# Performance work log

Hardware: AMD Instinct MI355X
Metric: run time of the kernel (lower is better)

The kernel has to match this reference:

```python
import jax, jax.numpy as jnp
import numpy as np

B, S, D, H, L, V, DFF = 2, 2048, 1024, 16, 4, 32000, 4096
DH = D // H
STD = 0.02
EPS = 1e-5


def _sinusoidal_pe(seq_len, d_model):
    pos = np.arange(seq_len)[:, None].astype(np.float32)
    div = np.exp(np.arange(0, d_model, 2).astype(np.float32) * (-np.log(10000.0) / d_model))
    pe = np.zeros((seq_len, d_model), dtype=np.float32)
    pe[:, 0::2] = np.sin(pos * div)
    pe[:, 1::2] = np.cos(pos * div)
    return jnp.asarray(pe)


def _layernorm(x, g, b):
    mu = jnp.mean(x, axis=-1, keepdims=True)
    var = jnp.mean(jnp.square(x - mu), axis=-1, keepdims=True)
    return (x - mu) * jax.lax.rsqrt(var + EPS) * g + b


def setup_inputs() -> dict:
    key = jax.random.key(0)
    ks = jax.random.split(key, 12)
    input_ids = jax.random.randint(ks[0], (B, S), 0, V)
    tok_emb = STD * jax.random.normal(ks[1], (V, D), dtype=jnp.float32)
    tok_emb = tok_emb.at[0].set(0.0)  # padding_idx=0 zeroed
    Wq = STD * jax.random.normal(ks[2], (L, D, D), dtype=jnp.float32)
    Wk = STD * jax.random.normal(ks[3], (L, D, D), dtype=jnp.float32)
    Wv = STD * jax.random.normal(ks[4], (L, D, D), dtype=jnp.float32)
    Wo = STD * jax.random.normal(ks[5], (L, D, D), dtype=jnp.float32)
    W1 = STD * jax.random.normal(ks[6], (L, D, DFF), dtype=jnp.float32)
    W2 = STD * jax.random.normal(ks[7], (L, DFF, D), dtype=jnp.float32)
    Wout = STD * jax.random.normal(ks[8], (D, V), dtype=jnp.float32)
    zD = jnp.zeros((L, D), dtype=jnp.float32)
    return {
        'input_ids': input_ids, 'tok_emb': tok_emb,
        'Wq': Wq, 'bq': zD, 'Wk': Wk, 'bk': zD, 'Wv': Wv, 'bv': zD, 'Wo': Wo, 'bo': zD,
        'ln1_g': jnp.ones((L, D), jnp.float32), 'ln1_b': zD,
        'W1': W1, 'b1': jnp.zeros((L, DFF), jnp.float32), 'W2': W2, 'b2': zD,
        'ln3_g': jnp.ones((L, D), jnp.float32), 'ln3_b': zD,
        'Wout': Wout, 'bout': jnp.zeros((V,), jnp.float32),
    }


def reference(input_ids, tok_emb, Wq, bq, Wk, bk, Wv, bv, Wo, bo,
              ln1_g, ln1_b, W1, b1, W2, b2, ln3_g, ln3_b, Wout, bout):
    pe = _sinusoidal_pe(S, D)
    causal = jnp.tril(jnp.ones((S, S), dtype=bool))  # [S,S]
    x = tok_emb[input_ids] * jnp.float32(np.sqrt(D)) + pe  # [B,S,D]
    scale = jnp.float32(1.0 / np.sqrt(DH))
    for l in range(L):
        q = (x @ Wq[l] + bq[l]).reshape(B, S, H, DH).transpose(0, 2, 1, 3)
        k = (x @ Wk[l] + bk[l]).reshape(B, S, H, DH).transpose(0, 2, 1, 3)
        v = (x @ Wv[l] + bv[l]).reshape(B, S, H, DH).transpose(0, 2, 1, 3)
        scores = jnp.einsum('bhqd,bhkd->bhqk', q, k) * scale
        scores = jnp.where(causal, scores, jnp.float32(-1e9))
        attn = jax.nn.softmax(scores, axis=-1)
        o = jnp.einsum('bhqk,bhkd->bhqd', attn, v)
        o = o.transpose(0, 2, 1, 3).reshape(B, S, D) @ Wo[l] + bo[l]
        x = _layernorm(x + o, ln1_g[l], ln1_b[l])
        f = jax.nn.relu(x @ W1[l] + b1[l]) @ W2[l] + b2[l]
        x = _layernorm(x + f, ln3_g[l], ln3_b[l])
    logits = x @ Wout + bout  # [B,S,V]
    return logits
```

## Files before the change

### kernel.cpp

```cpp
#include <hip/hip_runtime.h>
#include <stdint.h>

typedef unsigned short u16;
typedef __attribute__((ext_vector_type(8))) short bf16x8;
typedef __attribute__((ext_vector_type(4))) float f32x4;

#define NB 2
#define NS 2048
#define ND 1024
#define NH 16
#define NL 4
#define NV 32000
#define NF 4096
#define NDH 64
#define NM (NB*NS)

__device__ __forceinline__ u16 f2b(float f) {
  union { float f; uint32_t u; } v; v.f = f;
  uint32_t r = v.u + 0x7FFFu + ((v.u >> 16) & 1u);
  return (u16)(r >> 16);
}

#define GLOAD_LDS16(gp, lp) __builtin_amdgcn_global_load_lds( \
    (const __attribute__((address_space(1))) void*)(gp), \
    (__attribute__((address_space(3))) void*)(lp), 16, 0, 0)

#define VMCNT8 do { asm volatile("s_waitcnt vmcnt(8)" ::: "memory"); __builtin_amdgcn_sched_barrier(0); } while (0)
#define VMCNT0 do { asm volatile("s_waitcnt vmcnt(0)" ::: "memory"); __builtin_amdgcn_sched_barrier(0); } while (0)
#define LGKM0  do { asm volatile("s_waitcnt lgkmcnt(0)" ::: "memory"); __builtin_amdgcn_sched_barrier(0); } while (0)

__global__ __launch_bounds__(256)
void k_transpose_convert(const float* __restrict__ w, u16* __restrict__ wt, int K, int N) {
  __shared__ float tile[32][33];
  int n0 = blockIdx.x * 32;
  int k0 = blockIdx.y * 32;
  int tx = threadIdx.x & 31;
  int ty = threadIdx.x >> 5;
#pragma unroll
  for (int i = 0; i < 4; i++) {
    int kk = ty + i * 8;
    tile[kk][tx] = w[(size_t)(k0 + kk) * N + (n0 + tx)];
  }
  __syncthreads();
#pragma unroll
  for (int i = 0; i < 4; i++) {
    int nn = ty + i * 8;
    wt[(size_t)(n0 + nn) * K + (k0 + tx)] = f2b(tile[tx][nn]);
  }
}

__global__ __launch_bounds__(256)
void k_embed(const int* __restrict__ ids, const float* __restrict__ emb,
             float* __restrict__ x, u16* __restrict__ xb) {
  int row = blockIdx.x;
  int s = row & (NS - 1);
  int tok = ids[row];
  const float* e = emb + (size_t)tok * ND;
  int d0 = threadIdx.x * 4;
  float y[4];
#pragma unroll
  for (int j = 0; j < 4; j++) {
    int dd = d0 + j;
    float di = (float)(dd & ~1);
    float dv = expf(di * (-9.210340371976184f / (float)ND));
    float ang = (float)s * dv;
    float pe = (dd & 1) ? cosf(ang) : sinf(ang);
    y[j] = e[dd] * 32.0f + pe;
  }
  float4 w; w.x = y[0]; w.y = y[1]; w.z = y[2]; w.w = y[3];
  *(float4*)(x + (size_t)row * ND + d0) = w;
  uint2 pk;
  pk.x = (uint32_t)f2b(y[0]) | ((uint32_t)f2b(y[1]) << 16);
  pk.y = (uint32_t)f2b(y[2]) | ((uint32_t)f2b(y[3]) << 16);
  *(uint2*)(xb + (size_t)row * ND + d0) = pk;
}

__global__ __launch_bounds__(256)
void k_ln(const float* __restrict__ xin, const float* __restrict__ add,
          const float* __restrict__ g, const float* __restrict__ bb,
          float* __restrict__ xout, u16* __restrict__ xbout) {
  int row = blockIdx.x;
  int t = threadIdx.x;
  const float4 xi = *(const float4*)(xin + (size_t)row * ND + t * 4);
  const float4 ai = *(const float4*)(add + (size_t)row * ND + t * 4);
  float v0 = xi.x + ai.x, v1 = xi.y + ai.y, v2 = xi.z + ai.z, v3 = xi.w + ai.w;
  float s = v0 + v1 + v2 + v3;
  float s2 = v0 * v0 + v1 * v1 + v2 * v2 + v3 * v3;
#pragma unroll
  for (int d = 32; d >= 1; d >>= 1) { s += __shfl_xor(s, d); s2 += __shfl_xor(s2, d); }
  __shared__ float rs[8];
  int w = t >> 6;
  if ((t & 63) == 0) { rs[w] = s; rs[4 + w] = s2; }
  __syncthreads();
  s = rs[0] + rs[1] + rs[2] + rs[3];
  s2 = rs[4] + rs[5] + rs[6] + rs[7];
  float mu = s * (1.0f / ND);
  float var = s2 * (1.0f / ND) - mu * mu;
  float rr = rsqrtf(var + 1e-5f);
  const float4 gg = *(const float4*)(g + t * 4);
  const float4 be = *(const float4*)(bb + t * 4);
  float y0 = (v0 - mu) * rr * gg.x + be.x;
  float y1 = (v1 - mu) * rr * gg.y + be.y;
  float y2 = (v2 - mu) * rr * gg.z + be.z;
  float y3 = (v3 - mu) * rr * gg.w + be.w;
  float4 yo; yo.x = y0; yo.y = y1; yo.z = y2; yo.w = y3;
  *(float4*)(xout + (size_t)row * ND + t * 4) = yo;
  uint2 pk;
  pk.x = (uint32_t)f2b(y0) | ((uint32_t)f2b(y1) << 16);
  pk.y = (uint32_t)f2b(y2) | ((uint32_t)f2b(y3) << 16);
  *(uint2*)(xbout + (size_t)row * ND + t * 4) = pk;
}

template<int MODE>
__global__ __launch_bounds__(256)
void k_gemm_bt(const u16* __restrict__ A, const u16* __restrict__ Bt,
               const float* __restrict__ bias0, const float* __restrict__ bias1,
               const float* __restrict__ bias2,
               float* __restrict__ Cf, u16* __restrict__ Cb,
               int M, int N, int K, float scale) {
  constexpr int BM = 128, BN = 128, BK = 32;
  __shared__ __align__(16) u16 As[2][BM * BK];
  __shared__ __align__(16) u16 Bs[2][BN * BK];

  const int tid = threadIdx.x;
  const int lane = tid & 63;
  const int wave = tid >> 6;

  const int bm = blockIdx.x * BM;
  const int bn = blockIdx.y * BN;

  const int wr = (wave >> 1) * 64;
  const int wc = (wave & 1) * 64;
  const int lr = lane & 15;
  const int lk = (lane >> 4) * 8;

  const u16* Abase = A + (size_t)bm * K;
  const u16* Bbase = Bt + (size_t)bn * K;
  const int srow = lane >> 2;
  const int scol = (lane & 3) * 8;

  auto stage = [&](int buf, int kt) {
    const u16* Ag = Abase + (size_t)kt * BK + scol;
    const u16* Bg = Bbase + (size_t)kt * BK + scol;
#pragma unroll
    for (int i = 0; i < 2; i++) {
      const int rbase = (i * 4 + wave) * 16;
      GLOAD_LDS16(Ag + (size_t)(rbase + srow) * K, &As[buf][rbase * BK]);
      GLOAD_LDS16(Bg + (size_t)(rbase + srow) * K, &Bs[buf][rbase * BK]);
    }
  };

  f32x4 acc[4][4] = {};
  const int nk = K / BK;
  stage(0, 0);
  for (int kt = 0; kt < nk; ++kt) {
    __syncthreads();
    if (kt + 1 < nk) stage((kt + 1) & 1, kt + 1);
    const int buf = kt & 1;
    bf16x8 af[4], bfv[4];
#pragma unroll
    for (int m = 0; m < 4; m++)
      af[m] = *(const bf16x8*)(&As[buf][(wr + m * 16 + lr) * BK + lk]);
#pragma unroll
    for (int n = 0; n < 4; n++)
      bfv[n] = *(const bf16x8*)(&Bs[buf][(wc + n * 16 + lr) * BK + lk]);
#pragma unroll
    for (int m = 0; m < 4; m++)
#pragma unroll
      for (int n = 0; n < 4; n++)
        acc[m][n] = __builtin_amdgcn_mfma_f32_16x16x32_bf16(af[m], bfv[n], acc[m][n], 0, 0, 0);
  }

  const int lg = lane >> 4;
#pragma unroll
  for (int m = 0; m < 4; m++) {
#pragma unroll
    for (int n = 0; n < 4; n++) {
      int col = bn + wc + n * 16 + lr;
      float bv;
      if (MODE == 3) {
        int which = col >> 10;
        int cc = col & 1023;
        const float* bp = (which == 0) ? bias0 : ((which == 1) ? bias1 : bias2);
        bv = bp[cc];
      } else {
        bv = bias0[col];
      }
      if (MODE == 3 && (col >> 10) == 2) {
        int cc = col & 1023;
        int row0 = bm + wr + m * 16 + lg * 4;
        int b_ = row0 >> 11;
        int s_ = row0 & (NS - 1);
        int h_ = cc >> 6;
        int dh = cc & 63;
        ushort4 pk;
        pk.x = f2b(acc[m][n][0] + bv);
        pk.y = f2b(acc[m][n][1] + bv);
        pk.z = f2b(acc[m][n][2] + bv);
        pk.w = f2b(acc[m][n][3] + bv);
        *(ushort4*)(Cb + (size_t)2 * NM * ND +
                    ((((size_t)b_ * NH + h_) * NDH) + dh) * NS + s_) = pk;
        continue;
      }
#pragma unroll
      for (int j = 0; j < 4; j++) {
        int row = bm + wr + m * 16 + lg * 4 + j;
        float v = acc[m][n][j] + bv;
        if (MODE == 0) {
          Cf[(size_t)row * N + col] = v;
        } else if (MODE == 1) {
          Cb[(size_t)row * N + col] = f2b(fmaxf(v, 0.0f));
        } else {
          int which = col >> 10;
          int cc = col & 1023;
          if (which == 0) v *= scale;
          int b_ = row >> 11;
          int s_ = row & (NS - 1);
          int h_ = cc >> 6;
          int dh = cc & 63;
          Cb[(size_t)which * ((size_t)NM * ND) +
             ((((size_t)b_ * NH + h_) * NS) + s_) * NDH + dh] = f2b(v);
        }
      }
    }
  }
}

template<int MODE>
__global__ __launch_bounds__(512, 2)
void k_gemm256(const u16* __restrict__ A, const u16* __restrict__ Bt,
               const float* __restrict__ bias,
               float* __restrict__ Cf, u16* __restrict__ Cb,
               int M, int N, int K) {
  __shared__ __align__(16) u16 As2[2][256 * 64];
  __shared__ __align__(16) u16 Bs2[2][256 * 64];

  const int tid = threadIdx.x;
  const int lane = tid & 63;
  const int wave = tid >> 6;
  const int wrM = wave >> 2;
  const int wcN = wave & 3;
  const int lr = lane & 15;
  const int g = lane >> 4;
  const int r7 = lr & 7;

  const int bm = blockIdx.x * 256;
  const int bn = blockIdx.y * 256;

  const int srow_in = lane >> 3;
  const int schunk = lane & 7;
  const int sq = (schunk ^ srow_in) * 8;

  auto stageT = [&](int buf, int t) {
#pragma unroll
    for (int s = 0; s < 4; ++s) {
      const int rbase = (s * 8 + wave) * 8;
      const int row = rbase + srow_in;
      GLOAD_LDS16(A + (size_t)(bm + row) * K + t * 64 + sq, &As2[buf][rbase * 64]);
      GLOAD_LDS16(Bt + (size_t)(bn + row) * K + t * 64 + sq, &Bs2[buf][rbase * 64]);
    }
  };

  f32x4 acc[8][4] = {};
  const int NT = K / 64;

  stageT(0, 0);
  stageT(1, 1);

  for (int t = 0; t < NT; ++t) {
    const int buf = t & 1;
    if (t == NT - 1) { VMCNT0; } else { VMCNT8; }
    __builtin_amdgcn_s_barrier();

    const char* ab = (const char*)(&As2[buf][0]);
    const char* bb = (const char*)(&Bs2[buf][0]);
    bf16x8 aF[8], bF[4];
#pragma unroll
    for (int n = 0; n < 4; n++) {
      int row = wcN * 64 + n * 16 + lr;
      bF[n] = *(const bf16x8*)(bb + row * 128 + ((g ^ r7) * 16));
    }
#pragma unroll
    for (int m = 0; m < 8; m++) {
      int row = wrM * 128 + m * 16 + lr;
      aF[m] = *(const bf16x8*)(ab + row * 128 + ((g ^ r7) * 16));
    }
    __builtin_amdgcn_s_setprio(1);
#pragma unroll
    for (int m = 0; m < 8; m++)
#pragma unroll
      for (int n = 0; n < 4; n++)
        acc[m][n] = __builtin_amdgcn_mfma_f32_16x16x32_bf16(aF[m], bF[n], acc[m][n], 0, 0, 0);
    __builtin_amdgcn_s_setprio(0);

    bf16x8 aG[8], bG[4];
#pragma unroll
    for (int n = 0; n < 4; n++) {
      int row = wcN * 64 + n * 16 + lr;
      bG[n] = *(const bf16x8*)(bb + row * 128 + (((4 + g) ^ r7) * 16));
    }
#pragma unroll
    for (int m = 0; m < 8; m++) {
      int row = wrM * 128 + m * 16 + lr;
      aG[m] = *(const bf16x8*)(ab + row * 128 + (((4 + g) ^ r7) * 16));
    }
    LGKM0;
    __builtin_amdgcn_s_barrier();
    if (t + 2 < NT) stageT(buf, t + 2);
    __builtin_amdgcn_s_setprio(1);
#pragma unroll
    for (int m = 0; m < 8; m++)
#pragma unroll
      for (int n = 0; n < 4; n++)
        acc[m][n] = __builtin_amdgcn_mfma_f32_16x16x32_bf16(aG[m], bG[n], acc[m][n], 0, 0, 0);
    __builtin_amdgcn_s_setprio(0);
  }

#pragma unroll
  for (int m = 0; m < 8; m++) {
#pragma unroll
    for (int n = 0; n < 4; n++) {
      int col = bn + wcN * 64 + n * 16 + lr;
      float bv = bias[col];
#pragma unroll
      for (int j = 0; j < 4; j++) {
        int row = bm + wrM * 128 + m * 16 + g * 4 + j;
        float v = acc[m][n][j] + bv;
        if (MODE == 0) Cf[(size_t)row * N + col] = v;
        else           Cb[(size_t)row * N + col] = f2b(fmaxf(v, 0.0f));
      }
    }
  }
}

__global__ __launch_bounds__(256)
void k_attn(const u16* __restrict__ Q, const u16* __restrict__ Kq,
            const u16* __restrict__ Vt, u16* __restrict__ O) {
  const int qt = blockIdx.x;
  const int bh = blockIdx.y;
  const int b_ = bh >> 4, h_ = bh & 15;
  const int tid = threadIdx.x, lane = tid & 63, wave = tid >> 6;
  const int lr = lane & 15, lg = lane >> 4;

  __shared__ __align__(16) u16 Ks[64 * 64];
  __shared__ __align__(16) u16 Vs[64 * 64];
  __shared__ __align__(16) u16 Ps[4][16 * 64];

  const size_t base = (size_t)bh * NS * NDH;
  bf16x8 qf0, qf1;
  {
    const u16* qp = Q + base + (size_t)(qt * 64 + wave * 16 + lr) * NDH;
    qf0 = *(const bf16x8*)(qp + lg * 8);
    qf1 = *(const bf16x8*)(qp + 32 + lg * 8);
  }

  const int idx0 = tid, idx1 = tid + 256;
  const int r0 = idx0 >> 3, r1 = idx1 >> 3;
  const int c0 = (idx0 & 7) * 8, c1 = (idx1 & 7) * 8;
  const int so0 = r0 * 128 + ((c0 * 2) ^ ((r0 & 7) << 4));
  const int so1 = r1 * 128 + ((c1 * 2) ^ ((r1 & 7) << 4));

  bf16x8 rk0, rk1, rv0, rv1;
  auto loadregs = [&](int kt2) {
    const u16* Kg = Kq + base + (size_t)(kt2 * 64) * NDH;
    const u16* Vg = Vt + base + kt2 * 64;
    rk0 = *(const bf16x8*)(Kg + (size_t)r0 * NDH + c0);
    rk1 = *(const bf16x8*)(Kg + (size_t)r1 * NDH + c1);
    rv0 = *(const bf16x8*)(Vg + (size_t)r0 * NS + c0);
    rv1 = *(const bf16x8*)(Vg + (size_t)r1 * NS + c1);
  };

  float mrun[4] = {-1e30f, -1e30f, -1e30f, -1e30f};
  float lrun[4] = {0.f, 0.f, 0.f, 0.f};
  f32x4 oacc[4] = {};
  const int q0 = qt * 64 + wave * 16;

  loadregs(0);
  for (int kt2 = 0; kt2 <= qt; ++kt2) {
    *(bf16x8*)((char*)Ks + so0) = rk0;
    *(bf16x8*)((char*)Ks + so1) = rk1;
    *(bf16x8*)((char*)Vs + so0) = rv0;
    *(bf16x8*)((char*)Vs + so1) = rv1;
    __syncthreads();
    if (kt2 < qt) loadregs(kt2 + 1);

    f32x4 sc[4];
    __builtin_amdgcn_s_setprio(1);
#pragma unroll
    for (int c = 0; c < 4; c++) {
      int row = c * 16 + lr;
      const char* kp = (const char*)Ks + row * 128;
      int sm = (row & 7) << 4;
      bf16x8 k0 = *(const bf16x8*)(kp + ((lg * 16) ^ sm));
      bf16x8 k1 = *(const bf16x8*)(kp + ((64 + lg * 16) ^ sm));
      f32x4 s = {};
      s = __builtin_amdgcn_mfma_f32_16x16x32_bf16(qf0, k0, s, 0, 0, 0);
      s = __builtin_amdgcn_mfma_f32_16x16x32_bf16(qf1, k1, s, 0, 0, 0);
      sc[c] = s;
    }
    __builtin_amdgcn_s_setprio(0);

    if (kt2 == qt) {
#pragma unroll
      for (int c = 0; c < 4; c++)
#pragma unroll
        for (int j = 0; j < 4; j++) {
          int qg = q0 + lg * 4 + j;
          int kg = qt * 64 + c * 16 + lr;
          if (kg > qg) sc[c][j] = -1e9f;
        }
    }

#pragma unroll
    for (int j = 0; j < 4; j++) {
      float mt = fmaxf(fmaxf(sc[0][j], sc[1][j]), fmaxf(sc[2][j], sc[3][j]));
#pragma unroll
      for (int d = 8; d >= 1; d >>= 1) mt = fmaxf(mt, __shfl_xor(mt, d));
      float mnew = fmaxf(mrun[j], mt);
      float corr = __expf(mrun[j] - mnew);
      float ps = 0.f;
#pragma unroll
      for (int c = 0; c < 4; c++) {
        float p = __expf(sc[c][j] - mnew);
        sc[c][j] = p;
        ps += p;
      }
#pragma unroll
      for (int d = 8; d >= 1; d >>= 1) ps += __shfl_xor(ps, d);
      lrun[j] = lrun[j] * corr + ps;
      mrun[j] = mnew;
#pragma unroll
      for (int n = 0; n < 4; n++) oacc[n][j] *= corr;
    }

    char* pw = (char*)Ps[wave];
#pragma unroll
    for (int c = 0; c < 4; c++)
#pragma unroll
      for (int j = 0; j < 4; j++) {
        int row = lg * 4 + j;
        *(u16*)(pw + row * 128 + ((((c * 16 + lr) * 2)) ^ ((row & 7) << 4))) = f2b(sc[c][j]);
      }

    {
      int smq = (lr & 7) << 4;
      bf16x8 pa0 = *(const bf16x8*)(pw + lr * 128 + ((lg * 16) ^ smq));
      bf16x8 pa1 = *(const bf16x8*)(pw + lr * 128 + ((64 + lg * 16) ^ smq));
      __builtin_amdgcn_s_setprio(1);
#pragma unroll
      for (int n = 0; n < 4; n++) {
        int row = n * 16 + lr;
        const char* vp = (const char*)Vs + row * 128;
        int sm = (row & 7) << 4;
        bf16x8 v0 = *(const bf16x8*)(vp + ((lg * 16) ^ sm));
        bf16x8 v1 = *(const bf16x8*)(vp + ((64 + lg * 16) ^ sm));
        oacc[n] = __builtin_amdgcn_mfma_f32_16x16x32_bf16(pa0, v0, oacc[n], 0, 0, 0);
        oacc[n] = __builtin_amdgcn_mfma_f32_16x16x32_bf16(pa1, v1, oacc[n], 0, 0, 0);
      }
      __builtin_amdgcn_s_setprio(0);
    }
    __syncthreads();
  }

#pragma unroll
  for (int j = 0; j < 4; j++) {
    float inv = 1.0f / lrun[j];
    int s_ = qt * 64 + wave * 16 + lg * 4 + j;
    size_t orow = ((size_t)b_ * NS + s_) * ND + h_ * NDH;
#pragma unroll
    for (int n = 0; n < 4; n++)
      O[orow + n * 16 + lr] = f2b(oacc[n][j] * inv);
  }
}

extern "C" void kernel_launch(void* const* d_in, const int* in_sizes, int n_in,
                              void* d_out, int out_size, void* d_ws, size_t ws_size,
                              hipStream_t stream) {
  const int* ids = (const int*)d_in[0];
  const float* tok_emb = (const float*)d_in[1];
  const float* Wq = (const float*)d_in[2];
  const float* bq = (const float*)d_in[3];
  const float* Wk = (const float*)d_in[4];
  const float* bk = (const float*)d_in[5];
  const float* Wv = (const float*)d_in[6];
  const float* bv = (const float*)d_in[7];
  const float* Wo = (const float*)d_in[8];
  const float* bo = (const float*)d_in[9];
  const float* ln1g = (const float*)d_in[10];
  const float* ln1b = (const float*)d_in[11];
  const float* W1 = (const float*)d_in[12];
  const float* b1 = (const float*)d_in[13];
  const float* W2 = (const float*)d_in[14];
  const float* b2 = (const float*)d_in[15];
  const float* ln3g = (const float*)d_in[16];
  const float* ln3b = (const float*)d_in[17];
  const float* Wout = (const float*)d_in[18];
  const float* bout = (const float*)d_in[19];
  float* out = (float*)d_out;

  char* ws = (char*)d_ws;
  size_t off = 0;
  auto alloc = [&](size_t bytes) -> void* {
    void* p = ws + off;
    off += (bytes + 255) & ~(size_t)255;
    return p;
  };
  float* x    = (float*)alloc((size_t)NM * ND * 4);
  float* tmp  = (float*)alloc((size_t)NM * ND * 4);
  u16* xb     = (u16*)alloc((size_t)NM * ND * 2);
  u16* hb     = (u16*)alloc((size_t)NM * NF * 2);
  u16* qkvb   = (u16*)alloc((size_t)3 * NM * ND * 2);
  u16* ob     = (u16*)alloc((size_t)NM * ND * 2);
  u16* Wqkvt  = (u16*)alloc((size_t)NL * 3 * ND * ND * 2);
  u16* Wot    = (u16*)alloc((size_t)NL * ND * ND * 2);
  u16* W1t    = (u16*)alloc((size_t)NL * (size_t)NF * ND * 2);
  u16* W2t    = (u16*)alloc((size_t)NL * (size_t)ND * NF * 2);
  u16* Woutt  = (u16*)alloc((size_t)NV * ND * 2);

  for (int l = 0; l < NL; l++) {
    size_t wl = (size_t)l * ND * ND;
    u16* qkvl = Wqkvt + (size_t)l * 3 * ND * ND;
    dim3 gdd(ND / 32, ND / 32);
    k_transpose_convert<<<gdd, 256, 0, stream>>>(Wq + wl, qkvl, ND, ND);
    k_transpose_convert<<<gdd, 256, 0, stream>>>(Wk + wl, qkvl + (size_t)ND * ND, ND, ND);
    k_transpose_convert<<<gdd, 256, 0, stream>>>(Wv + wl, qkvl + (size_t)2 * ND * ND, ND, ND);
    k_transpose_convert<<<gdd, 256, 0, stream>>>(Wo + wl, Wot + wl, ND, ND);
    k_transpose_convert<<<dim3(NF / 32, ND / 32), 256, 0, stream>>>(
        W1 + (size_t)l * ND * NF, W1t + (size_t)l * (size_t)NF * ND, ND, NF);
    k_transpose_convert<<<dim3(ND / 32, NF / 32), 256, 0, stream>>>(
        W2 + (size_t)l * NF * ND, W2t + (size_t)l * (size_t)ND * NF, NF, ND);
  }
  k_transpose_convert<<<dim3(NV / 32, ND / 32), 256, 0, stream>>>(Wout, Woutt, ND, NV);

  k_embed<<<NM, 256, 0, stream>>>(ids, tok_emb, x, xb);

  for (int l = 0; l < NL; l++) {
    size_t wl = (size_t)l * ND * ND;
    u16* qkvl = Wqkvt + (size_t)l * 3 * ND * ND;

    k_gemm_bt<3><<<dim3(NM / 128, 3 * ND / 128), 256, 0, stream>>>(
        xb, qkvl, bq + l * ND, bk + l * ND, bv + l * ND,
        nullptr, qkvb, NM, 3 * ND, ND, 0.125f);

    k_attn<<<dim3(NS / 64, NB * NH), 256, 0, stream>>>(
        qkvb, qkvb + (size_t)NM * ND, qkvb + (size_t)2 * NM * ND, ob);

    k_gemm_bt<0><<<dim3(NM / 128, ND / 128), 256, 0, stream>>>(
        ob, Wot + wl, bo + l * ND, nullptr, nullptr, tmp, nullptr, NM, ND, ND, 1.0f);

    k_ln<<<NM, 256, 0, stream>>>(x, tmp, ln1g + l * ND, ln1b + l * ND, x, xb);

    k_gemm256<1><<<dim3(NM / 256, NF / 256), 512, 0, stream>>>(
        xb, W1t + (size_t)l * (size_t)NF * ND, b1 + l * NF, nullptr, hb, NM, NF, ND);

    k_gemm_bt<0><<<dim3(NM / 128, ND / 128), 256, 0, stream>>>(
        hb, W2t + (size_t)l * (size_t)ND * NF, b2 + l * ND, nullptr, nullptr,
        tmp, nullptr, NM, ND, NF, 1.0f);

    k_ln<<<NM, 256, 0, stream>>>(x, tmp, ln3g + l * ND, ln3b + l * ND, x, xb);
  }

  k_gemm256<0><<<dim3(NM / 256, NV / 256), 512, 0, stream>>>(
      xb, Woutt, bout, out, nullptr, NM, NV, ND);
}
```

Before: 1.882 ms.

## Restructure 256-tile GEMM into quadrant phases and enlarge attention query tile

The 256x256 GEMM main loop is split into four quadrant phases. Each phase loads only the A/B fragments it needs, uses extra barriers, and interleaves the next-tile A and B global-to-LDS stages between MFMA phases, which lowers register pressure and spreads memory issue. The attention kernel now processes 128 queries per block (32 per wave), so each K/V tile staged in LDS is reused by twice as many queries and half as many blocks are launched. It also adds a lazy softmax rescale that skips the correction unless the running max grows by more than 8. The trade-offs are more barriers in the GEMM, coarser causal load balancing in attention, and fewer attention blocks to fill the GPU.

```diff
diff --git a/kernel.cpp b/kernel.cpp
--- a/kernel.cpp
+++ b/kernel.cpp
@@ -28,6 +28,7 @@
 #define VMCNT8 do { asm volatile("s_waitcnt vmcnt(8)" ::: "memory"); __builtin_amdgcn_sched_barrier(0); } while (0)
 #define VMCNT0 do { asm volatile("s_waitcnt vmcnt(0)" ::: "memory"); __builtin_amdgcn_sched_barrier(0); } while (0)
 #define LGKM0  do { asm volatile("s_waitcnt lgkmcnt(0)" ::: "memory"); __builtin_amdgcn_sched_barrier(0); } while (0)
+#define MFMA16(a,b,c) __builtin_amdgcn_mfma_f32_16x16x32_bf16((a),(b),(c),0,0,0)
 
 __global__ __launch_bounds__(256)
 void k_transpose_convert(const float* __restrict__ w, u16* __restrict__ wt, int K, int N) {
@@ -168,7 +169,7 @@
     for (int m = 0; m < 4; m++)
 #pragma unroll
       for (int n = 0; n < 4; n++)
-        acc[m][n] = __builtin_amdgcn_mfma_f32_16x16x32_bf16(af[m], bfv[n], acc[m][n], 0, 0, 0);
+        acc[m][n] = MFMA16(af[m], bfv[n], acc[m][n]);
   }
 
   const int lg = lane >> 4;
@@ -251,69 +252,112 @@
   const int schunk = lane & 7;
   const int sq = (schunk ^ srow_in) * 8;
 
-  auto stageT = [&](int buf, int t) {
-#pragma unroll
-    for (int s = 0; s < 4; ++s) {
-      const int rbase = (s * 8 + wave) * 8;
-      const int row = rbase + srow_in;
-      GLOAD_LDS16(A + (size_t)(bm + row) * K + t * 64 + sq, &As2[buf][rbase * 64]);
-      GLOAD_LDS16(Bt + (size_t)(bn + row) * K + t * 64 + sq, &Bs2[buf][rbase * 64]);
+  auto stageA = [&](int buf, int t) {
+#pragma unroll
+    for (int s2 = 0; s2 < 4; ++s2) {
+      const int rbase = (s2 * 8 + wave) * 8;
+      GLOAD_LDS16(A + (size_t)(bm + rbase + srow_in) * K + t * 64 + sq, &As2[buf][rbase * 64]);
+    }
+  };
+  auto stageB = [&](int buf, int t) {
+#pragma unroll
+    for (int s2 = 0; s2 < 4; ++s2) {
+      const int rbase = (s2 * 8 + wave) * 8;
+      GLOAD_LDS16(Bt + (size_t)(bn + rbase + srow_in) * K + t * 64 + sq, &Bs2[buf][rbase * 64]);
     }
   };
 
   f32x4 acc[8][4] = {};
   const int NT = K / 64;
 
-  stageT(0, 0);
-  stageT(1, 1);
+  stageA(0, 0); stageB(0, 0);
+  stageA(1, 1); stageB(1, 1);
 
   for (int t = 0; t < NT; ++t) {
     const int buf = t & 1;
-    if (t == NT - 1) { VMCNT0; } else { VMCNT8; }
+    if (t + 1 < NT) { VMCNT8; } else { VMCNT0; }
     __builtin_amdgcn_s_barrier();
 
     const char* ab = (const char*)(&As2[buf][0]);
-    const char* bb = (const char*)(&Bs2[buf][0]);
-    bf16x8 aF[8], bF[4];
-#pragma unroll
-    for (int n = 0; n < 4; n++) {
+    const char* bb2 = (const char*)(&Bs2[buf][0]);
+    bf16x8 aF[4][2], bF[4][2];
+
+#pragma unroll
+    for (int m = 0; m < 4; m++) {
+      int row = wrM * 128 + m * 16 + lr;
+      aF[m][0] = *(const bf16x8*)(ab + row * 128 + ((g ^ r7) * 16));
+      aF[m][1] = *(const bf16x8*)(ab + row * 128 + (((4 + g) ^ r7) * 16));
+    }
+#pragma unroll
+    for (int n = 0; n < 2; n++) {
       int row = wcN * 64 + n * 16 + lr;
-      bF[n] = *(const bf16x8*)(bb + row * 128 + ((g ^ r7) * 16));
-    }
-#pragma unroll
-    for (int m = 0; m < 8; m++) {
-      int row = wrM * 128 + m * 16 + lr;
-      aF[m] = *(const bf16x8*)(ab + row * 128 + ((g ^ r7) * 16));
-    }
+      bF[n][0] = *(const bf16x8*)(bb2 + row * 128 + ((g ^ r7) * 16));
+      bF[n][1] = *(const bf16x8*)(bb2 + row * 128 + (((4 + g) ^ r7) * 16));
+    }
+    __builtin_amdgcn_s_barrier();
+    LGKM0;
     __builtin_amdgcn_s_setprio(1);
 #pragma unroll
-    for (int m = 0; m < 8; m++)
-#pragma unroll
-      for (int n = 0; n < 4; n++)
-        acc[m][n] = __builtin_amdgcn_mfma_f32_16x16x32_bf16(aF[m], bF[n], acc[m][n], 0, 0, 0);
+    for (int m = 0; m < 4; m++)
+#pragma unroll
+      for (int n = 0; n < 2; n++) {
+        acc[m][n] = MFMA16(aF[m][0], bF[n][0], acc[m][n]);
+        acc[m][n] = MFMA16(aF[m][1], bF[n][1], acc[m][n]);
+      }
     __builtin_amdgcn_s_setprio(0);
-
-    bf16x8 aG[8], bG[4];
-#pragma unroll
-    for (int n = 0; n < 4; n++) {
+    __builtin_amdgcn_s_barrier();
+
+#pragma unroll
+    for (int n = 2; n < 4; n++) {
       int row = wcN * 64 + n * 16 + lr;
-      bG[n] = *(const bf16x8*)(bb + row * 128 + (((4 + g) ^ r7) * 16));
-    }
-#pragma unroll
-    for (int m = 0; m < 8; m++) {
-      int row = wrM * 128 + m * 16 + lr;
-      aG[m] = *(const bf16x8*)(ab + row * 128 + (((4 + g) ^ r7) * 16));
-    }
+      bF[n][0] = *(const bf16x8*)(bb2 + row * 128 + ((g ^ r7) * 16));
+      bF[n][1] = *(const bf16x8*)(bb2 + row * 128 + (((4 + g) ^ r7) * 16));
+    }
+    __builtin_amdgcn_s_barrier();
     LGKM0;
-    __builtin_amdgcn_s_barrier();
-    if (t + 2 < NT) stageT(buf, t + 2);
     __builtin_amdgcn_s_setprio(1);
 #pragma unroll
-    for (int m = 0; m < 8; m++)
-#pragma unroll
-      for (int n = 0; n < 4; n++)
-        acc[m][n] = __builtin_amdgcn_mfma_f32_16x16x32_bf16(aG[m], bG[n], acc[m][n], 0, 0, 0);
+    for (int m = 0; m < 4; m++)
+#pragma unroll
+      for (int n = 2; n < 4; n++) {
+        acc[m][n] = MFMA16(aF[m][0], bF[n][0], acc[m][n]);
+        acc[m][n] = MFMA16(aF[m][1], bF[n][1], acc[m][n]);
+      }
     __builtin_amdgcn_s_setprio(0);
+    __builtin_amdgcn_s_barrier();
+
+#pragma unroll
+    for (int m = 0; m < 4; m++) {
+      int row = wrM * 128 + (m + 4) * 16 + lr;
+      aF[m][0] = *(const bf16x8*)(ab + row * 128 + ((g ^ r7) * 16));
+      aF[m][1] = *(const bf16x8*)(ab + row * 128 + (((4 + g) ^ r7) * 16));
+    }
+    if (t + 2 < NT) stageB(buf, t + 2);
+    __builtin_amdgcn_s_barrier();
+    LGKM0;
+    __builtin_amdgcn_s_setprio(1);
+#pragma unroll
+    for (int m = 0; m < 4; m++)
+#pragma unroll
+      for (int n = 0; n < 2; n++) {
+        acc[m + 4][n] = MFMA16(aF[m][0], bF[n][0], acc[m + 4][n]);
+        acc[m + 4][n] = MFMA16(aF[m][1], bF[n][1], acc[m + 4][n]);
+      }
+    __builtin_amdgcn_s_setprio(0);
+    __builtin_amdgcn_s_barrier();
+
+    if (t + 2 < NT) stageA(buf, t + 2);
+    __builtin_amdgcn_s_barrier();
+    __builtin_amdgcn_s_setprio(1);
+#pragma unroll
+    for (int m = 0; m < 4; m++)
+#pragma unroll
+      for (int n = 2; n < 4; n++) {
+        acc[m + 4][n] = MFMA16(aF[m][0], bF[n][0], acc[m + 4][n]);
+        acc[m + 4][n] = MFMA16(aF[m][1], bF[n][1], acc[m + 4][n]);
+      }
+    __builtin_amdgcn_s_setprio(0);
+    __builtin_amdgcn_s_barrier();
   }
 
 #pragma unroll
@@ -344,14 +388,15 @@
 
   __shared__ __align__(16) u16 Ks[64 * 64];
   __shared__ __align__(16) u16 Vs[64 * 64];
-  __shared__ __align__(16) u16 Ps[4][16 * 64];
+  __shared__ __align__(16) u16 Ps[4][32 * 64];
 
   const size_t base = (size_t)bh * NS * NDH;
-  bf16x8 qf0, qf1;
-  {
-    const u16* qp = Q + base + (size_t)(qt * 64 + wave * 16 + lr) * NDH;
-    qf0 = *(const bf16x8*)(qp + lg * 8);
-    qf1 = *(const bf16x8*)(qp + 32 + lg * 8);
+  bf16x8 qf[2][2];
+#pragma unroll
+  for (int mf = 0; mf < 2; mf++) {
+    const u16* qp = Q + base + (size_t)(qt * 128 + wave * 32 + mf * 16 + lr) * NDH;
+    qf[mf][0] = *(const bf16x8*)(qp + lg * 8);
+    qf[mf][1] = *(const bf16x8*)(qp + 32 + lg * 8);
   }
 
   const int idx0 = tid, idx1 = tid + 256;
@@ -370,82 +415,119 @@
     rv1 = *(const bf16x8*)(Vg + (size_t)r1 * NS + c1);
   };
 
-  float mrun[4] = {-1e30f, -1e30f, -1e30f, -1e30f};
-  float lrun[4] = {0.f, 0.f, 0.f, 0.f};
-  f32x4 oacc[4] = {};
-  const int q0 = qt * 64 + wave * 16;
+  float mrun[2][4], lrun[2][4];
+  f32x4 oacc[2][4] = {};
+#pragma unroll
+  for (int mf = 0; mf < 2; mf++)
+#pragma unroll
+    for (int j = 0; j < 4; j++) { mrun[mf][j] = -1e30f; lrun[mf][j] = 0.f; }
+
+  const int qmin = qt * 128 + wave * 32;
+  const int qmax = qmin + 31;
+  const int nkv = 2 * qt + 2;
 
   loadregs(0);
-  for (int kt2 = 0; kt2 <= qt; ++kt2) {
+  for (int kt2 = 0; kt2 < nkv; ++kt2) {
     *(bf16x8*)((char*)Ks + so0) = rk0;
     *(bf16x8*)((char*)Ks + so1) = rk1;
     *(bf16x8*)((char*)Vs + so0) = rv0;
     *(bf16x8*)((char*)Vs + so1) = rv1;
     __syncthreads();
-    if (kt2 < qt) loadregs(kt2 + 1);
-
-    f32x4 sc[4];
-    __builtin_amdgcn_s_setprio(1);
-#pragma unroll
-    for (int c = 0; c < 4; c++) {
-      int row = c * 16 + lr;
-      const char* kp = (const char*)Ks + row * 128;
-      int sm = (row & 7) << 4;
-      bf16x8 k0 = *(const bf16x8*)(kp + ((lg * 16) ^ sm));
-      bf16x8 k1 = *(const bf16x8*)(kp + ((64 + lg * 16) ^ sm));
-      f32x4 s = {};
-      s = __builtin_amdgcn_mfma_f32_16x16x32_bf16(qf0, k0, s, 0, 0, 0);
-      s = __builtin_amdgcn_mfma_f32_16x16x32_bf16(qf1, k1, s, 0, 0, 0);
-      sc[c] = s;
-    }
-    __builtin_amdgcn_s_setprio(0);
-
-    if (kt2 == qt) {
-#pragma unroll
-      for (int c = 0; c < 4; c++)
+    if (kt2 + 1 < nkv) loadregs(kt2 + 1);
+
+    const bool active = (kt2 * 64 <= qmax);
+    if (active) {
+      f32x4 sc[2][4];
+      __builtin_amdgcn_s_setprio(1);
+#pragma unroll
+      for (int c = 0; c < 4; c++) {
+        int row = c * 16 + lr;
+        const char* kp = (const char*)Ks + row * 128;
+        int sm = (row & 7) << 4;
+        bf16x8 k0 = *(const bf16x8*)(kp + ((lg * 16) ^ sm));
+        bf16x8 k1 = *(const bf16x8*)(kp + ((64 + lg * 16) ^ sm));
+#pragma unroll
+        for (int mf = 0; mf < 2; mf++) {
+          f32x4 s = {};
+          s = MFMA16(qf[mf][0], k0, s);
+          s = MFMA16(qf[mf][1], k1, s);
+          sc[mf][c] = s;
+        }
+      }
+      __builtin_amdgcn_s_setprio(0);
+
+      if (kt2 * 64 + 63 > qmin) {
+#pragma unroll
+        for (int mf = 0; mf < 2; mf++)
+#pragma unroll
+          for (int c = 0; c < 4; c++)
+#pragma unroll
+            for (int j = 0; j < 4; j++) {
+              int qg = qmin + mf * 16 + lg * 4 + j;
+              int kg = kt2 * 64 + c * 16 + lr;
+              if (kg > qg) sc[mf][c][j] = -1e9f;
+            }
+      }
+
+      float mt[2][4];
+      float dmax = -1e30f;
+#pragma unroll
+      for (int mf = 0; mf < 2; mf++)
 #pragma unroll
         for (int j = 0; j < 4; j++) {
-          int qg = q0 + lg * 4 + j;
-          int kg = qt * 64 + c * 16 + lr;
-          if (kg > qg) sc[c][j] = -1e9f;
+          float m0 = fmaxf(fmaxf(sc[mf][0][j], sc[mf][1][j]), fmaxf(sc[mf][2][j], sc[mf][3][j]));
+#pragma unroll
+          for (int d = 8; d >= 1; d >>= 1) m0 = fmaxf(m0, __shfl_xor(m0, d));
+          mt[mf][j] = m0;
+          dmax = fmaxf(dmax, m0 - mrun[mf][j]);
         }
-    }
-
-#pragma unroll
-    for (int j = 0; j < 4; j++) {
-      float mt = fmaxf(fmaxf(sc[0][j], sc[1][j]), fmaxf(sc[2][j], sc[3][j]));
-#pragma unroll
-      for (int d = 8; d >= 1; d >>= 1) mt = fmaxf(mt, __shfl_xor(mt, d));
-      float mnew = fmaxf(mrun[j], mt);
-      float corr = __expf(mrun[j] - mnew);
-      float ps = 0.f;
-#pragma unroll
-      for (int c = 0; c < 4; c++) {
-        float p = __expf(sc[c][j] - mnew);
-        sc[c][j] = p;
-        ps += p;
-      }
-#pragma unroll
-      for (int d = 8; d >= 1; d >>= 1) ps += __shfl_xor(ps, d);
-      lrun[j] = lrun[j] * corr + ps;
-      mrun[j] = mnew;
-#pragma unroll
-      for (int n = 0; n < 4; n++) oacc[n][j] *= corr;
-    }
-
-    char* pw = (char*)Ps[wave];
-#pragma unroll
-    for (int c = 0; c < 4; c++)
-#pragma unroll
-      for (int j = 0; j < 4; j++) {
-        int row = lg * 4 + j;
-        *(u16*)(pw + row * 128 + ((((c * 16 + lr) * 2)) ^ ((row & 7) << 4))) = f2b(sc[c][j]);
-      }
-
-    {
-      int smq = (lr & 7) << 4;
-      bf16x8 pa0 = *(const bf16x8*)(pw + lr * 128 + ((lg * 16) ^ smq));
-      bf16x8 pa1 = *(const bf16x8*)(pw + lr * 128 + ((64 + lg * 16) ^ smq));
+      const bool need = __any(dmax > 8.0f);
+
+#pragma unroll
+      for (int mf = 0; mf < 2; mf++)
+#pragma unroll
+        for (int j = 0; j < 4; j++) {
+          float mold = mrun[mf][j];
+          float mnew = need ? fmaxf(mold, mt[mf][j]) : mold;
+          float ps = 0.f;
+#pragma unroll
+          for (int c = 0; c < 4; c++) {
+            float p = __expf(sc[mf][c][j] - mnew);
+            sc[mf][c][j] = p;
+            ps += p;
+          }
+#pragma unroll
+          for (int d = 8; d >= 1; d >>= 1) ps += __shfl_xor(ps, d);
+          if (need) {
+            float corr = __expf(mold - mnew);
+            lrun[mf][j] = lrun[mf][j] * corr + ps;
+            mrun[mf][j] = mnew;
+#pragma unroll
+            for (int n = 0; n < 4; n++) oacc[mf][n][j] *= corr;
+          } else {
+            lrun[mf][j] += ps;
+          }
+        }
+
+      char* pw = (char*)Ps[wave];
+#pragma unroll
+      for (int mf = 0; mf < 2; mf++)
+#pragma unroll
+        for (int c = 0; c < 4; c++)
+#pragma unroll
+          for (int j = 0; j < 4; j++) {
+            int row = mf * 16 + lg * 4 + j;
+            *(u16*)(pw + row * 128 + ((((c * 16 + lr) * 2)) ^ ((row & 7) << 4))) = f2b(sc[mf][c][j]);
+          }
+
+      bf16x8 pa[2][2];
+#pragma unroll
+      for (int mf = 0; mf < 2; mf++) {
+        int prow = mf * 16 + lr;
+        int smq = (prow & 7) << 4;
+        pa[mf][0] = *(const bf16x8*)(pw + prow * 128 + ((lg * 16) ^ smq));
+        pa[mf][1] = *(const bf16x8*)(pw + prow * 128 + ((64 + lg * 16) ^ smq));
+      }
       __builtin_amdgcn_s_setprio(1);
 #pragma unroll
       for (int n = 0; n < 4; n++) {
@@ -454,8 +536,11 @@
         int sm = (row & 7) << 4;
         bf16x8 v0 = *(const bf16x8*)(vp + ((lg * 16) ^ sm));
         bf16x8 v1 = *(const bf16x8*)(vp + ((64 + lg * 16) ^ sm));
-        oacc[n] = __builtin_amdgcn_mfma_f32_16x16x32_bf16(pa0, v0, oacc[n], 0, 0, 0);
-        oacc[n] = __builtin_amdgcn_mfma_f32_16x16x32_bf16(pa1, v1, oacc[n], 0, 0, 0);
+#pragma unroll
+        for (int mf = 0; mf < 2; mf++) {
+          oacc[mf][n] = MFMA16(pa[mf][0], v0, oacc[mf][n]);
+          oacc[mf][n] = MFMA16(pa[mf][1], v1, oacc[mf][n]);
+        }
       }
       __builtin_amdgcn_s_setprio(0);
     }
@@ -463,14 +548,16 @@
   }
 
 #pragma unroll
-  for (int j = 0; j < 4; j++) {
-    float inv = 1.0f / lrun[j];
-    int s_ = qt * 64 + wave * 16 + lg * 4 + j;
-    size_t orow = ((size_t)b_ * NS + s_) * ND + h_ * NDH;
-#pragma unroll
-    for (int n = 0; n < 4; n++)
-      O[orow + n * 16 + lr] = f2b(oacc[n][j] * inv);
-  }
+  for (int mf = 0; mf < 2; mf++)
+#pragma unroll
+    for (int j = 0; j < 4; j++) {
+      float inv = 1.0f / lrun[mf][j];
+      int s_ = qt * 128 + wave * 32 + mf * 16 + lg * 4 + j;
+      size_t orow = ((size_t)b_ * NS + s_) * ND + h_ * NDH;
+#pragma unroll
+      for (int n = 0; n < 4; n++)
+        O[orow + n * 16 + lr] = f2b(oacc[mf][n][j] * inv);
+    }
 }
 
 extern "C" void kernel_launch(void* const* d_in, const int* in_sizes, int n_in,
@@ -542,7 +629,7 @@
         xb, qkvl, bq + l * ND, bk + l * ND, bv + l * ND,
         nullptr, qkvb, NM, 3 * ND, ND, 0.125f);
 
-    k_attn<<<dim3(NS / 64, NB * NH), 256, 0, stream>>>(
+    k_attn<<<dim3(NS / 128, NB * NH), 256, 0, stream>>>(
         qkvb, qkvb + (size_t)NM * ND, qkvb + (size_t)2 * NM * ND, ob);
 
     k_gemm_bt<0><<<dim3(NM / 128, ND / 128), 256, 0, stream>>>(
```

Result: slower. 2.317 ms (+23.1%).
